# Optimization experiments

Hardware: AMD Instinct MI355X
Metric: run time of the kernel (lower is better)

Reference implementation:

```python
import jax, jax.numpy as jnp
import numpy as np

B = 2          # batch
S = 4096       # byte-level sequence length
D = 512        # d_hidden_bytelevel
BPL = 4        # bytes_per_latent
H = 16         # n_attention_heads
DQK = 64       # d_qkv_bytelevel (== rope d_hidden)
DLAT = 1024    # d_hidden_latent
LQ = S // BPL  # latent sequence length
EPS = 1.1920929e-07  # torch RMSNorm default eps = float32 finfo eps
ROPE_BASE = 10000.0


def _rope(x, pos):
    # x: [B, H, L, DQK], pos: [L] float positions. Half-split rotation.
    half = DQK // 2
    inv_freq = ROPE_BASE ** (-jnp.arange(half, dtype=jnp.float32) / half)  # [half]
    ang = pos[:, None] * inv_freq[None, :]                                 # [L, half]
    cos, sin = jnp.cos(ang), jnp.sin(ang)
    x1, x2 = x[..., :half], x[..., half:]
    return jnp.concatenate([x1 * cos - x2 * sin, x1 * sin + x2 * cos], axis=-1)


def setup_inputs() -> dict:
    key = jax.random.key(0)
    ks = jax.random.split(key, 9)
    s = 0.02
    return {
        "x": jax.random.normal(ks[0], (B, S, D), dtype=jnp.float32),
        "norm_w": jnp.ones((D,), dtype=jnp.float32),
        "wq_w": jax.random.normal(ks[1], (BPL * D, H * DQK), dtype=jnp.float32) * s,
        "wq_b": jax.random.normal(ks[2], (H * DQK,), dtype=jnp.float32) * s,
        "wkv_w": jax.random.normal(ks[3], (D, 2 * H * DQK), dtype=jnp.float32) * s,
        "wkv_b": jax.random.normal(ks[4], (2 * H * DQK,), dtype=jnp.float32) * s,
        "wout_w": jax.random.normal(ks[5], (H * DQK, DLAT), dtype=jnp.float32) * s,
        "wout_b": jax.random.normal(ks[6], (DLAT,), dtype=jnp.float32) * s,
        "wbyp_w": jax.random.normal(ks[7], (BPL * D, DLAT), dtype=jnp.float32) * s,
    }


def reference(x, norm_w, wq_w, wq_b, wkv_w, wkv_b, wout_w, wout_b, wbyp_w):
    # RMSNorm (elementwise affine)
    normalized = x * jax.lax.rsqrt(jnp.mean(x * x, axis=-1, keepdims=True) + EPS) * norm_w
    # merge groups of BPL bytes -> latent query tokens: [B, LQ, BPL*D]
    merged = normalized.reshape(B, LQ, BPL * D)
    # fused Q projection: [B, H, LQ, DQK]
    q = (merged @ wq_w + wq_b).reshape(B, LQ, H, DQK).transpose(0, 2, 1, 3)
    # merged KV projection: split dim first, then heads -> [B, S, 2, H, DQK]
    kv = (normalized @ wkv_w + wkv_b).reshape(B, S, 2, H, DQK)
    k = kv[:, :, 0].transpose(0, 2, 1, 3)  # [B, H, S, DQK]
    v = kv[:, :, 1].transpose(0, 2, 1, 3)
    # strided RoPE for Q (positions i*BPL), unit-stride for K
    q = _rope(q, jnp.arange(LQ, dtype=jnp.float32) * BPL)
    k = _rope(k, jnp.arange(S, dtype=jnp.float32))
    # SDPA (non-causal)
    scores = jnp.einsum('bhqd,bhkd->bhqk', q, k) * (1.0 / np.sqrt(DQK).astype(np.float32))
    attn = jax.nn.softmax(scores, axis=-1)
    attn_out = jnp.einsum('bhqk,bhkd->bhqd', attn, v)
    attn_concat = attn_out.transpose(0, 2, 1, 3).reshape(B, LQ, H * DQK)
    out = attn_concat @ wout_w + wout_b
    # bypass: raw x grouped by BPL, bias-free projection
    bypass = x.reshape(B, LQ, BPL * D) @ wbyp_w
    return out + bypass
```

## Files before the change

### kernel.cpp

```cpp
#include <hip/hip_runtime.h>

using u16 = unsigned short;
using u32 = unsigned int;

typedef __attribute__((ext_vector_type(8))) short bf16x8;
typedef __attribute__((ext_vector_type(8))) unsigned short u16x8;
typedef __attribute__((ext_vector_type(4))) float f32x4;
typedef __attribute__((ext_vector_type(16))) float f32x16;
typedef __attribute__((ext_vector_type(4))) u32 u32x4;

constexpr int Bb   = 2;
constexpr int Ss   = 4096;
constexpr int Dd   = 512;
constexpr int Hh   = 16;
constexpr int DQK  = 64;
constexpr int LQ   = 1024;
constexpr int DLAT = 1024;

#define QSCL 0.18033688011112042f

__device__ __forceinline__ u16 f2bf(float f){
  u32 u = __float_as_uint(f);
  u += 0x7FFFu + ((u >> 16) & 1u);
  return (u16)(u >> 16);
}
__device__ __forceinline__ u32 permpack(float hi, float lo){
  return __builtin_amdgcn_perm(__float_as_uint(hi), __float_as_uint(lo), 0x07060302u);
}

#define GLDS16(gp, lp) \
  __builtin_amdgcn_global_load_lds((const __attribute__((address_space(1))) u32*)(gp), \
                                   (__attribute__((address_space(3))) u32*)(lp), 16, 0, 0)

__global__ __launch_bounds__(256) void rmsnorm_kernel(
    const float* __restrict__ x, const float* __restrict__ w,
    u16* __restrict__ normb, u16* __restrict__ xb)
{
  const int lane = threadIdx.x & 63;
  const int row  = blockIdx.x * 4 + (threadIdx.x >> 6);
  const float4* xr = (const float4*)(x + (size_t)row * Dd);
  float4 a = xr[lane*2], b2 = xr[lane*2 + 1];
  float ss = a.x*a.x + a.y*a.y + a.z*a.z + a.w*a.w
           + b2.x*b2.x + b2.y*b2.y + b2.z*b2.z + b2.w*b2.w;
  #pragma unroll
  for (int off = 1; off < 64; off <<= 1) ss += __shfl_xor(ss, off);
  const float sc = rsqrtf(ss * (1.0f / Dd) + 1.1920929e-07f);
  const int c0 = lane * 8;
  const float4* wr4 = (const float4*)(w + c0);
  float4 w0 = wr4[0], w1 = wr4[1];
  u16x8 nv, xv;
  nv[0]=f2bf(a.x *sc*w0.x); nv[1]=f2bf(a.y *sc*w0.y); nv[2]=f2bf(a.z *sc*w0.z); nv[3]=f2bf(a.w *sc*w0.w);
  nv[4]=f2bf(b2.x*sc*w1.x); nv[5]=f2bf(b2.y*sc*w1.y); nv[6]=f2bf(b2.z*sc*w1.z); nv[7]=f2bf(b2.w*sc*w1.w);
  xv[0]=f2bf(a.x);  xv[1]=f2bf(a.y);  xv[2]=f2bf(a.z);  xv[3]=f2bf(a.w);
  xv[4]=f2bf(b2.x); xv[5]=f2bf(b2.y); xv[6]=f2bf(b2.z); xv[7]=f2bf(b2.w);
  *(u16x8*)(normb + (size_t)row * Dd + c0) = nv;
  *(u16x8*)(xb    + (size_t)row * Dd + c0) = xv;
}

__global__ __launch_bounds__(256) void rope_tab_kernel(float2* __restrict__ tab){
  int i = blockIdx.x * 256 + threadIdx.x;
  int pos = i >> 5, d = i & 31;
  float inv = exp2f(-(float)d * 0.41524101186092028f);
  float ang = (float)pos * inv;
  float s, c;
  sincosf(ang, &s, &c);
  tab[i] = make_float2(c, s);
}

__global__ __launch_bounds__(256) void transpose_cast_kernel(
    const float* __restrict__ W, u16* __restrict__ Wt,
    int N, int ldt, int koff)
{
  __shared__ float t[64][65];
  const int k0 = blockIdx.x * 64, n0 = blockIdx.y * 64;
  const int c = threadIdx.x & 63, r0 = threadIdx.x >> 6;
  #pragma unroll
  for (int i = 0; i < 16; ++i){
    int r = i*4 + r0;
    t[r][c] = W[(size_t)(k0 + r) * N + n0 + c];
  }
  __syncthreads();
  #pragma unroll
  for (int i = 0; i < 16; ++i){
    int r = i*4 + r0;
    Wt[(size_t)(n0 + r) * ldt + koff + k0 + c] = f2bf(t[c][r]);
  }
}

__device__ __forceinline__ void gemm_core64(
    const u16* __restrict__ A, int lda,
    const u16* __restrict__ Bt, int ldb, int kofs,
    int K, int bm0, int bn0, char* lds,
    f32x4 (&acc)[4])
{
  const int tid = threadIdx.x, lane = tid & 63, w = tid >> 6;
  const int l15 = lane & 15, l4 = lane >> 4;

  #pragma unroll
  for (int j = 0; j < 4; ++j) acc[j] = (f32x4){0.f, 0.f, 0.f, 0.f};

  auto stage = [&](int t){
    char* dst = lds + (t % 3) * 16384;
    const int k0 = t * 64;
    #pragma unroll
    for (int i = 0; i < 4; ++i){
      int u = i*256 + tid;
      int row = u >> 3;
      int colb = ((u & 7) * 16) ^ ((row & 7) << 4);
      const u16* src = (row < 64)
        ? A  + (size_t)(bm0 + row) * lda + k0 + (colb >> 1)
        : Bt + (size_t)(bn0 + row - 64) * ldb + kofs + k0 + (colb >> 1);
      GLDS16(src, dst + u*16);
    }
  };

  const int nt = K >> 6;
  stage(0);
  if (nt > 1) stage(1);

  #pragma unroll 1
  for (int t = 0; t < nt; ++t){
    if (t + 1 < nt) { asm volatile("s_waitcnt vmcnt(4)" ::: "memory"); }
    else            { asm volatile("s_waitcnt vmcnt(0)" ::: "memory"); }
    __builtin_amdgcn_sched_barrier(0);
    __builtin_amdgcn_s_barrier();

    const char* kb = lds + (t % 3) * 16384;
    bf16x8 af[2], bf[4][2];
    #pragma unroll
    for (int ks = 0; ks < 2; ++ks){
      const int row = w*16 + l15;
      af[ks] = *(const bf16x8*)(kb + row*128 + ((ks*64 + l4*16) ^ ((row & 7) << 4)));
    }
    #pragma unroll
    for (int j = 0; j < 4; ++j)
      #pragma unroll
      for (int ks = 0; ks < 2; ++ks){
        const int row = 64 + j*16 + l15;
        bf[j][ks] = *(const bf16x8*)(kb + row*128 + ((ks*64 + l4*16) ^ ((row & 7) << 4)));
      }
    asm volatile("s_waitcnt lgkmcnt(0)" ::: "memory");
    __builtin_amdgcn_sched_barrier(0);
    if (t + 2 < nt) stage(t + 2);

    __builtin_amdgcn_s_setprio(1);
    #pragma unroll
    for (int ks = 0; ks < 2; ++ks)
      #pragma unroll
      for (int j = 0; j < 4; ++j)
        acc[j] = __builtin_amdgcn_mfma_f32_16x16x32_bf16(af[ks], bf[j][ks], acc[j], 0, 0, 0);
    __builtin_amdgcn_s_setprio(0);
  }
}

__device__ __forceinline__ void gemm_core256(
    const u16* __restrict__ A, int lda, int ksplit,
    const u16* __restrict__ A2, int lda2,
    const u16* __restrict__ Bt, int ldb,
    int K, int bm0, int bn0, char* lds,
    f32x4 (&acc)[4][4])
{
  const int tid = threadIdx.x, lane = tid & 63, w = tid >> 6;
  const int wr = w >> 1, wc = w & 1;
  const int l15 = lane & 15, l4 = lane >> 4;

  #pragma unroll
  for (int i = 0; i < 4; ++i)
    #pragma unroll
    for (int j = 0; j < 4; ++j) acc[i][j] = (f32x4){0.f, 0.f, 0.f, 0.f};

  auto stage = [&](int t){
    char* dst = lds + (t % 3) * 49152;
    const int k0 = t * 64;
    #pragma unroll
    for (int i = 0; i < 6; ++i){
      int u = i*512 + tid;
      int row = u >> 3;
      int colb = ((u & 7) * 16) ^ ((row & 7) << 4);
      const u16* src;
      if (row < 256){
        if (k0 < ksplit) src = A  + (size_t)(bm0 + row) * lda  + k0 + (colb >> 1);
        else             src = A2 + (size_t)(bm0 + row) * lda2 + (k0 - ksplit) + (colb >> 1);
      } else {
        src = Bt + (size_t)(bn0 + row - 256) * ldb + k0 + (colb >> 1);
      }
      GLDS16(src, dst + u*16);
    }
  };

  const int nt = K >> 6;
  stage(0);
  if (nt > 1) stage(1);

  #pragma unroll 1
  for (int t = 0; t < nt; ++t){
    if (t + 1 < nt) { asm volatile("s_waitcnt vmcnt(6)" ::: "memory"); }
    else            { asm volatile("s_waitcnt vmcnt(0)" ::: "memory"); }
    __builtin_amdgcn_sched_barrier(0);
    __builtin_amdgcn_s_barrier();

    const char* kb = lds + (t % 3) * 49152;
    bf16x8 af[4][2], bf[4][2];
    #pragma unroll
    for (int i = 0; i < 4; ++i)
      #pragma unroll
      for (int ks = 0; ks < 2; ++ks){
        const int row = wr*64 + i*16 + l15;
        af[i][ks] = *(const bf16x8*)(kb + row*128 + ((ks*64 + l4*16) ^ ((row & 7) << 4)));
      }
    #pragma unroll
    for (int j = 0; j < 4; ++j)
      #pragma unroll
      for (int ks = 0; ks < 2; ++ks){
        const int row = 256 + wc*64 + j*16 + l15;
        bf[j][ks] = *(const bf16x8*)(kb + row*128 + ((ks*64 + l4*16) ^ ((row & 7) << 4)));
      }
    asm volatile("s_waitcnt lgkmcnt(0)" ::: "memory");
    __builtin_amdgcn_sched_barrier(0);
    if (t + 2 < nt) stage(t + 2);

    __builtin_amdgcn_s_setprio(1);
    #pragma unroll
    for (int ks = 0; ks < 2; ++ks)
      #pragma unroll
      for (int i = 0; i < 4; ++i)
        #pragma unroll
        for (int j = 0; j < 4; ++j)
          acc[i][j] = __builtin_amdgcn_mfma_f32_16x16x32_bf16(af[i][ks], bf[j][ks], acc[i][j], 0, 0, 0);
    __builtin_amdgcn_s_setprio(0);
  }
}

__global__ __launch_bounds__(512, 1) void qkv_kernel(
    const u16* __restrict__ normb,
    const u16* __restrict__ wtq, const u16* __restrict__ wtkv,
    const float* __restrict__ wq_b, const float* __restrict__ wkv_b,
    const float2* __restrict__ rtab,
    u16* __restrict__ Qb, u16* __restrict__ Kb, u16* __restrict__ Vtb)
{
  __shared__ char lds[147456];
  const int bid = blockIdx.x;
  const int lane = threadIdx.x & 63, w = threadIdx.x >> 6;
  const int wr = w >> 1, wc = w & 1;
  const int ml = (lane >> 4) * 4, nl = lane & 15;
  f32x4 acc[4][4];

  if (bid < 64){
    const int bm0 = (bid & 7) * 256, bn0 = (bid >> 3) * 128;
    gemm_core256(normb, 2048, 2048, normb, 2048, wtq, 2048, 2048, bm0, bn0, lds, acc);
    const int nbase = bn0 + wc*64;
    const int h = nbase >> 6;
    #pragma unroll
    for (int i = 0; i < 4; ++i){
      #pragma unroll
      for (int j = 0; j < 2; ++j){
        const int d1 = j*16 + nl;
        const float b1 = wq_b[nbase + j*16 + nl], b2v = wq_b[nbase + (j+2)*16 + nl];
        #pragma unroll
        for (int r = 0; r < 4; ++r){
          int m = bm0 + wr*64 + i*16 + ml + r;
          int b = m >> 10, lq = m & 1023;
          float x1 = acc[i][j][r] + b1;
          float x2 = acc[i][j+2][r] + b2v;
          float2 cs = rtab[(lq*4)*32 + d1];
          size_t ob = ((size_t)(b*Hh + h) * LQ + lq) * DQK;
          Qb[ob + d1]      = f2bf((x1*cs.x - x2*cs.y) * QSCL);
          Qb[ob + d1 + 32] = f2bf((x1*cs.y + x2*cs.x) * QSCL);
        }
      }
    }
  } else {
    const int t = bid - 64;
    const int bm0 = (t & 31) * 256, bn0 = (t >> 5) * 128;
    gemm_core256(normb, 512, 512, normb, 512, wtkv, 512, 512, bm0, bn0, lds, acc);
    const int nbase = bn0 + wc*64;
    const int kv = nbase >> 10;
    const int h = (nbase & 1023) >> 6;
    #pragma unroll
    for (int i = 0; i < 4; ++i){
      const int m0 = bm0 + wr*64 + i*16 + ml;
      const int b = m0 >> 12, s = m0 & 4095;
      if (kv == 0){
        #pragma unroll
        for (int r = 0; r < 4; ++r){
          size_t ob = ((size_t)(b*Hh + h) * Ss + s + r) * DQK;
          #pragma unroll
          for (int j = 0; j < 2; ++j){
            int d1 = j*16 + nl;
            float x1 = acc[i][j][r]   + wkv_b[nbase + j*16 + nl];
            float x2 = acc[i][j+2][r] + wkv_b[nbase + (j+2)*16 + nl];
            float2 cs = rtab[(s+r)*32 + d1];
            Kb[ob + d1]      = f2bf(x1*cs.x - x2*cs.y);
            Kb[ob + d1 + 32] = f2bf(x1*cs.y + x2*cs.x);
          }
        }
      } else {
        #pragma unroll
        for (int j = 0; j < 4; ++j){
          const int d = j*16 + nl;
          const float bb = wkv_b[nbase + d];
          uint2 pv;
          pv.x = permpack(acc[i][j][1] + bb, acc[i][j][0] + bb);
          pv.y = permpack(acc[i][j][3] + bb, acc[i][j][2] + bb);
          *(uint2*)(Vtb + (((size_t)(b*Hh + h)) * DQK + d) * Ss + s) = pv;
        }
      }
    }
  }
}

__global__ __launch_bounds__(256, 3) void out_kernel(
    const u16* __restrict__ ACb, const u16* __restrict__ xb,
    const u16* __restrict__ wto, const float* __restrict__ wout_b,
    float* __restrict__ outp)
{
  __shared__ char lds[49152];
  const int bm0 = blockIdx.x * 64, bn0 = blockIdx.y * 64;
  const int lane = threadIdx.x & 63, w = threadIdx.x >> 6;
  const int ml = (lane >> 4) * 4, nl = lane & 15;
  f32x4 acc[4], acc2[4];
  gemm_core64(ACb, 1024, wto, 3072, 0,    1024, bm0, bn0, lds, acc);
  __syncthreads();
  gemm_core64(xb,  2048, wto, 3072, 1024, 2048, bm0, bn0, lds, acc2);
  #pragma unroll
  for (int j = 0; j < 4; ++j){
    const int n = bn0 + j*16 + nl;
    const float bb = wout_b[n];
    #pragma unroll
    for (int r = 0; r < 4; ++r){
      int m = bm0 + w*16 + ml + r;
      outp[(size_t)m * DLAT + n] = acc[j][r] + acc2[j][r] + bb;
    }
  }
}

__global__ __launch_bounds__(512, 2) void flash_kernel(
    const u16* __restrict__ Qg, const u16* __restrict__ Kg,
    const u16* __restrict__ Vtg, float* __restrict__ Opart,
    float* __restrict__ lpart)
{
  const int tid = threadIdx.x, lane = tid & 63, w = tid >> 6;
  const int bid = blockIdx.x;
  const int swz = (bid & 7) * 32 + (bid >> 3);
  const int sq = swz & 3, qh = (swz >> 2) & 1, bh = swz >> 3;
  const int sbase = sq * 1024;
  const int l31 = lane & 31, hgl = lane >> 5;

  __shared__ char lds[49152];

  bf16x8 qf[2][4];
  #pragma unroll
  for (int qt = 0; qt < 2; ++qt)
    #pragma unroll
    for (int ks = 0; ks < 4; ++ks)
      qf[qt][ks] = *(const bf16x8*)(Qg + ((size_t)bh*LQ + qh*512 + w*64 + qt*32 + l31) * DQK + ks*16 + hgl*8);

  f32x16 o[2][2];
  #pragma unroll
  for (int qt = 0; qt < 2; ++qt)
    #pragma unroll
    for (int nd = 0; nd < 2; ++nd)
      #pragma unroll
      for (int r = 0; r < 16; ++r) o[qt][nd][r] = 0.f;
  float l_run[2] = {0.f, 0.f};

  auto stage = [&](int t){
    char* dst = lds + (t % 3) * 16384;
    const int s0 = sbase + t * 64;
    #pragma unroll
    for (int i = 0; i < 2; ++i){
      int u = (w*2 + i) * 64 + lane;
      int row = (u >> 3) & 63;
      int colb = ((u & 7) * 16) ^ ((row & 7) << 4);
      const u16* src = (u < 512)
          ? Kg  + ((size_t)bh*Ss  + s0 + row) * DQK + (colb >> 1)
          : Vtg + ((size_t)bh*DQK + row) * Ss + s0  + (colb >> 1);
      GLDS16(src, dst + u*16);
    }
  };

  stage(0);
  stage(1);

  #pragma unroll 1
  for (int t = 0; t < 16; ++t){
    if (t < 15) { asm volatile("s_waitcnt vmcnt(2)" ::: "memory"); }
    else        { asm volatile("s_waitcnt vmcnt(0)" ::: "memory"); }
    __builtin_amdgcn_sched_barrier(0);
    __builtin_amdgcn_s_barrier();

    const char* kb = lds + (t % 3) * 16384;
    bf16x8 kf[2][4], vf[2][4];
    #pragma unroll
    for (int kvt = 0; kvt < 2; ++kvt)
      #pragma unroll
      for (int ks = 0; ks < 4; ++ks){
        const int row = kvt*32 + l31;
        kf[kvt][ks] = *(const bf16x8*)(kb + row*128 + ((ks*32 + hgl*16) ^ ((row & 7) << 4)));
      }
    #pragma unroll
    for (int nd = 0; nd < 2; ++nd)
      #pragma unroll
      for (int k2 = 0; k2 < 4; ++k2){
        const int row = nd*32 + l31;
        vf[nd][k2] = *(const bf16x8*)(kb + 8192 + row*128 + ((k2*32 + hgl*16) ^ ((row & 7) << 4)));
      }
    asm volatile("s_waitcnt lgkmcnt(0)" ::: "memory");
    __builtin_amdgcn_sched_barrier(0);
    if (t < 14) stage(t + 2);

    #pragma unroll
    for (int qt = 0; qt < 2; ++qt){
      f32x16 sc[2];
      #pragma unroll
      for (int kvt = 0; kvt < 2; ++kvt)
        #pragma unroll
        for (int r = 0; r < 16; ++r) sc[kvt][r] = 0.f;
      __builtin_amdgcn_s_setprio(1);
      #pragma unroll
      for (int kvt = 0; kvt < 2; ++kvt)
        #pragma unroll
        for (int ks = 0; ks < 4; ++ks)
          sc[kvt] = __builtin_amdgcn_mfma_f32_32x32x16_bf16(kf[kvt][ks], qf[qt][ks], sc[kvt], 0, 0, 0);
      __builtin_amdgcn_s_setprio(0);

      float s_loc = 0.f;
      u32x4 paw[4];
      #pragma unroll
      for (int kvt = 0; kvt < 2; ++kvt){
        #pragma unroll
        for (int r = 0; r < 16; ++r){
          float p = __builtin_amdgcn_exp2f(sc[kvt][r]);
          sc[kvt][r] = p;
          s_loc += p;
        }
        #pragma unroll
        for (int k2r = 0; k2r < 2; ++k2r){
          u32 a0 = permpack(sc[kvt][k2r*8+1], sc[kvt][k2r*8+0]);
          u32 a1 = permpack(sc[kvt][k2r*8+3], sc[kvt][k2r*8+2]);
          u32 a2 = permpack(sc[kvt][k2r*8+5], sc[kvt][k2r*8+4]);
          u32 a3 = permpack(sc[kvt][k2r*8+7], sc[kvt][k2r*8+6]);
          asm("v_permlane32_swap_b32 %0, %1" : "+v"(a0), "+v"(a2));
          asm("v_permlane32_swap_b32 %0, %1" : "+v"(a1), "+v"(a3));
          const int k2 = kvt*2 + k2r;
          paw[k2][0] = a0; paw[k2][1] = a1;
          paw[k2][2] = a2; paw[k2][3] = a3;
        }
      }
      l_run[qt] += s_loc;

      __builtin_amdgcn_s_setprio(1);
      #pragma unroll
      for (int nd = 0; nd < 2; ++nd)
        #pragma unroll
        for (int k2 = 0; k2 < 4; ++k2)
          o[qt][nd] = __builtin_amdgcn_mfma_f32_32x32x16_bf16(
              __builtin_bit_cast(bf16x8, paw[k2]), vf[nd][k2], o[qt][nd], 0, 0, 0);
      __builtin_amdgcn_s_setprio(0);
    }
  }

  #pragma unroll
  for (int qt = 0; qt < 2; ++qt){
    float lf = l_run[qt] + __shfl_xor(l_run[qt], 32);
    float* Ob = Opart + ((size_t)sq * 32768 + (size_t)bh * 1024) * 64;
    #pragma unroll
    for (int nd = 0; nd < 2; ++nd)
      #pragma unroll
      for (int r = 0; r < 16; ++r){
        int q = qh*512 + w*64 + qt*32 + (r & 3) + 8*(r >> 2) + 4*hgl;
        Ob[(size_t)q * 64 + nd*32 + l31] = o[qt][nd][r];
      }
    if (hgl == 0)
      lpart[(size_t)sq * 32768 + (size_t)bh * 1024 + qh*512 + w*64 + qt*32 + l31] = lf;
  }
}

__global__ __launch_bounds__(256) void merge_kernel(
    const float* __restrict__ Opart, const float* __restrict__ lpart,
    u16* __restrict__ AC)
{
  int idx = blockIdx.x * 256 + threadIdx.x;
  int row = idx >> 3, dg = idx & 7;
  int bh = row >> 10, lq = row & 1023;
  int b = bh >> 4, h = bh & 15;
  float a[8];
  #pragma unroll
  for (int e = 0; e < 8; ++e) a[e] = 0.f;
  float lt = 0.f;
  #pragma unroll
  for (int p = 0; p < 4; ++p){
    const float4* pp = (const float4*)(Opart + ((size_t)p * 32768 + row) * 64 + dg * 8);
    float4 v0 = pp[0], v1 = pp[1];
    a[0]+=v0.x; a[1]+=v0.y; a[2]+=v0.z; a[3]+=v0.w;
    a[4]+=v1.x; a[5]+=v1.y; a[6]+=v1.z; a[7]+=v1.w;
    lt += lpart[(size_t)p * 32768 + row];
  }
  float rl = 1.0f / lt;
  u16x8 r;
  #pragma unroll
  for (int e = 0; e < 8; ++e) r[e] = f2bf(a[e] * rl);
  *(u16x8*)(AC + ((size_t)(b*LQ + lq)) * (Hh*DQK) + h*DQK + dg*8) = r;
}

extern "C" void kernel_launch(void* const* d_in, const int* in_sizes, int n_in,
                              void* d_out, int out_size, void* d_ws, size_t ws_size,
                              hipStream_t stream)
{
  (void)in_sizes; (void)n_in; (void)out_size; (void)ws_size;
  const float* x      = (const float*)d_in[0];
  const float* norm_w = (const float*)d_in[1];
  const float* wq_w   = (const float*)d_in[2];
  const float* wq_b   = (const float*)d_in[3];
  const float* wkv_w  = (const float*)d_in[4];
  const float* wkv_b  = (const float*)d_in[5];
  const float* wout_w = (const float*)d_in[6];
  const float* wout_b = (const float*)d_in[7];
  const float* wbyp_w = (const float*)d_in[8];
  float* outp = (float*)d_out;

  char* p = (char*)d_ws;
  u16* normb = (u16*)p; p += (size_t)8192*512*2;
  u16* xb    = (u16*)p; p += (size_t)8192*512*2;
  u16* wtq   = (u16*)p; p += (size_t)1024*2048*2;
  u16* wtkv  = (u16*)p; p += (size_t)2048*512*2;
  u16* wto   = (u16*)p; p += (size_t)1024*3072*2;
  u16* Qb    = (u16*)p; p += (size_t)32*1024*64*2;
  u16* Kb    = (u16*)p; p += (size_t)32*4096*64*2;
  u16* Vtb   = (u16*)p; p += (size_t)32*64*4096*2;
  u16* ACb   = (u16*)p; p += (size_t)2048*1024*2;
  float2* rtab = (float2*)p; p += (size_t)4096*32*sizeof(float2);
  float* Opart = (float*)p; p += (size_t)4*32768*64*4;
  float* lpart = (float*)p; p += (size_t)4*32768*4;

  rmsnorm_kernel<<<2048, 256, 0, stream>>>(x, norm_w, normb, xb);
  rope_tab_kernel<<<512, 256, 0, stream>>>(rtab);
  transpose_cast_kernel<<<dim3(32,16), 256, 0, stream>>>(wq_w,   wtq,  1024, 2048, 0);
  transpose_cast_kernel<<<dim3(8,32),  256, 0, stream>>>(wkv_w,  wtkv, 2048, 512,  0);
  transpose_cast_kernel<<<dim3(16,16), 256, 0, stream>>>(wout_w, wto,  1024, 3072, 0);
  transpose_cast_kernel<<<dim3(32,16), 256, 0, stream>>>(wbyp_w, wto,  1024, 3072, 1024);

  qkv_kernel<<<576, 512, 0, stream>>>(normb, wtq, wtkv, wq_b, wkv_b, rtab, Qb, Kb, Vtb);
  flash_kernel<<<256, 512, 0, stream>>>(Qb, Kb, Vtb, Opart, lpart);
  merge_kernel<<<1024, 256, 0, stream>>>(Opart, lpart, ACb);
  out_kernel<<<dim3(32,16), 256, 0, stream>>>(ACb, xb, wto, wout_b, outp);
}
```

Baseline: 131.1 us.

## Fuse prep kernels, merge out GEMMs, bf16 partials, reorder flash score MFMAs

Six preprocessing launches (RMSNorm, RoPE table, four weight transpose-casts) become one kernel that branches on block index, which removes launch gaps. The output projection and bypass GEMMs now run as a single K-concatenated GEMM loop, so the accumulator and pipeline are shared. Flash partial outputs are stored in bf16, halving merge traffic at some precision cost. The flash loop computes score MFMAs for both query tiles before loading V fragments, and issues the next K/V prefetch earlier.

```diff
diff --git a/kernel.cpp b/kernel.cpp
--- a/kernel.cpp
+++ b/kernel.cpp
@@ -32,47 +32,11 @@
   __builtin_amdgcn_global_load_lds((const __attribute__((address_space(1))) u32*)(gp), \
                                    (__attribute__((address_space(3))) u32*)(lp), 16, 0, 0)
 
-__global__ __launch_bounds__(256) void rmsnorm_kernel(
-    const float* __restrict__ x, const float* __restrict__ w,
-    u16* __restrict__ normb, u16* __restrict__ xb)
-{
-  const int lane = threadIdx.x & 63;
-  const int row  = blockIdx.x * 4 + (threadIdx.x >> 6);
-  const float4* xr = (const float4*)(x + (size_t)row * Dd);
-  float4 a = xr[lane*2], b2 = xr[lane*2 + 1];
-  float ss = a.x*a.x + a.y*a.y + a.z*a.z + a.w*a.w
-           + b2.x*b2.x + b2.y*b2.y + b2.z*b2.z + b2.w*b2.w;
-  #pragma unroll
-  for (int off = 1; off < 64; off <<= 1) ss += __shfl_xor(ss, off);
-  const float sc = rsqrtf(ss * (1.0f / Dd) + 1.1920929e-07f);
-  const int c0 = lane * 8;
-  const float4* wr4 = (const float4*)(w + c0);
-  float4 w0 = wr4[0], w1 = wr4[1];
-  u16x8 nv, xv;
-  nv[0]=f2bf(a.x *sc*w0.x); nv[1]=f2bf(a.y *sc*w0.y); nv[2]=f2bf(a.z *sc*w0.z); nv[3]=f2bf(a.w *sc*w0.w);
-  nv[4]=f2bf(b2.x*sc*w1.x); nv[5]=f2bf(b2.y*sc*w1.y); nv[6]=f2bf(b2.z*sc*w1.z); nv[7]=f2bf(b2.w*sc*w1.w);
-  xv[0]=f2bf(a.x);  xv[1]=f2bf(a.y);  xv[2]=f2bf(a.z);  xv[3]=f2bf(a.w);
-  xv[4]=f2bf(b2.x); xv[5]=f2bf(b2.y); xv[6]=f2bf(b2.z); xv[7]=f2bf(b2.w);
-  *(u16x8*)(normb + (size_t)row * Dd + c0) = nv;
-  *(u16x8*)(xb    + (size_t)row * Dd + c0) = xv;
-}
-
-__global__ __launch_bounds__(256) void rope_tab_kernel(float2* __restrict__ tab){
-  int i = blockIdx.x * 256 + threadIdx.x;
-  int pos = i >> 5, d = i & 31;
-  float inv = exp2f(-(float)d * 0.41524101186092028f);
-  float ang = (float)pos * inv;
-  float s, c;
-  sincosf(ang, &s, &c);
-  tab[i] = make_float2(c, s);
-}
-
-__global__ __launch_bounds__(256) void transpose_cast_kernel(
+__device__ __forceinline__ void tc_body(
     const float* __restrict__ W, u16* __restrict__ Wt,
-    int N, int ldt, int koff)
-{
-  __shared__ float t[64][65];
-  const int k0 = blockIdx.x * 64, n0 = blockIdx.y * 64;
+    int N, int ldt, int koff, int k0, int n0, float* tbuf)
+{
+  float (*t)[65] = (float(*)[65])tbuf;
   const int c = threadIdx.x & 63, r0 = threadIdx.x >> 6;
   #pragma unroll
   for (int i = 0; i < 16; ++i){
@@ -87,9 +51,65 @@
   }
 }
 
+__global__ __launch_bounds__(256) void prep_kernel(
+    const float* __restrict__ x, const float* __restrict__ norm_w,
+    const float* __restrict__ wq_w, const float* __restrict__ wkv_w,
+    const float* __restrict__ wout_w, const float* __restrict__ wbyp_w,
+    u16* __restrict__ normb, u16* __restrict__ xb,
+    float2* __restrict__ rtab,
+    u16* __restrict__ wtq, u16* __restrict__ wtkv, u16* __restrict__ wto)
+{
+  __shared__ float tbuf[64*65];
+  const int bid = blockIdx.x;
+  if (bid < 2048){
+    const int lane = threadIdx.x & 63;
+    const int row  = bid * 4 + (threadIdx.x >> 6);
+    const float4* xr = (const float4*)(x + (size_t)row * Dd);
+    float4 a = xr[lane*2], b2 = xr[lane*2 + 1];
+    float ss = a.x*a.x + a.y*a.y + a.z*a.z + a.w*a.w
+             + b2.x*b2.x + b2.y*b2.y + b2.z*b2.z + b2.w*b2.w;
+    #pragma unroll
+    for (int off = 1; off < 64; off <<= 1) ss += __shfl_xor(ss, off);
+    const float sc = rsqrtf(ss * (1.0f / Dd) + 1.1920929e-07f);
+    const int c0 = lane * 8;
+    const float4* wr4 = (const float4*)(norm_w + c0);
+    float4 w0 = wr4[0], w1 = wr4[1];
+    u16x8 nv, xv;
+    nv[0]=f2bf(a.x *sc*w0.x); nv[1]=f2bf(a.y *sc*w0.y); nv[2]=f2bf(a.z *sc*w0.z); nv[3]=f2bf(a.w *sc*w0.w);
+    nv[4]=f2bf(b2.x*sc*w1.x); nv[5]=f2bf(b2.y*sc*w1.y); nv[6]=f2bf(b2.z*sc*w1.z); nv[7]=f2bf(b2.w*sc*w1.w);
+    xv[0]=f2bf(a.x);  xv[1]=f2bf(a.y);  xv[2]=f2bf(a.z);  xv[3]=f2bf(a.w);
+    xv[4]=f2bf(b2.x); xv[5]=f2bf(b2.y); xv[6]=f2bf(b2.z); xv[7]=f2bf(b2.w);
+    *(u16x8*)(normb + (size_t)row * Dd + c0) = nv;
+    *(u16x8*)(xb    + (size_t)row * Dd + c0) = xv;
+  } else if (bid < 2560){
+    int i = (bid - 2048) * 256 + threadIdx.x;
+    int pos = i >> 5, d = i & 31;
+    float inv = exp2f(-(float)d * 0.41524101186092028f);
+    float ang = (float)pos * inv;
+    float s, c;
+    sincosf(ang, &s, &c);
+    rtab[i] = make_float2(c, s);
+  } else {
+    int t = bid - 2560;
+    if (t < 512){
+      tc_body(wq_w, wtq, 1024, 2048, 0, (t & 31) * 64, (t >> 5) * 64, tbuf);
+    } else if (t < 768){
+      int u = t - 512;
+      tc_body(wkv_w, wtkv, 2048, 512, 0, (u & 7) * 64, (u >> 3) * 64, tbuf);
+    } else if (t < 1024){
+      int u = t - 768;
+      tc_body(wout_w, wto, 1024, 3072, 0, (u & 15) * 64, (u >> 4) * 64, tbuf);
+    } else {
+      int u = t - 1024;
+      tc_body(wbyp_w, wto, 1024, 3072, 1024, (u & 31) * 64, (u >> 5) * 64, tbuf);
+    }
+  }
+}
+
 __device__ __forceinline__ void gemm_core64(
-    const u16* __restrict__ A, int lda,
-    const u16* __restrict__ Bt, int ldb, int kofs,
+    const u16* __restrict__ A, int lda, int ksplit,
+    const u16* __restrict__ A2, int lda2,
+    const u16* __restrict__ Bt, int ldb,
     int K, int bm0, int bn0, char* lds,
     f32x4 (&acc)[4])
 {
@@ -107,9 +127,13 @@
       int u = i*256 + tid;
       int row = u >> 3;
       int colb = ((u & 7) * 16) ^ ((row & 7) << 4);
-      const u16* src = (row < 64)
-        ? A  + (size_t)(bm0 + row) * lda + k0 + (colb >> 1)
-        : Bt + (size_t)(bn0 + row - 64) * ldb + kofs + k0 + (colb >> 1);
+      const u16* src;
+      if (row < 64){
+        if (k0 < ksplit) src = A  + (size_t)(bm0 + row) * lda  + k0 + (colb >> 1);
+        else             src = A2 + (size_t)(bm0 + row) * lda2 + (k0 - ksplit) + (colb >> 1);
+      } else {
+        src = Bt + (size_t)(bn0 + row - 64) * ldb + k0 + (colb >> 1);
+      }
       GLDS16(src, dst + u*16);
     }
   };
@@ -318,10 +342,8 @@
   const int bm0 = blockIdx.x * 64, bn0 = blockIdx.y * 64;
   const int lane = threadIdx.x & 63, w = threadIdx.x >> 6;
   const int ml = (lane >> 4) * 4, nl = lane & 15;
-  f32x4 acc[4], acc2[4];
-  gemm_core64(ACb, 1024, wto, 3072, 0,    1024, bm0, bn0, lds, acc);
-  __syncthreads();
-  gemm_core64(xb,  2048, wto, 3072, 1024, 2048, bm0, bn0, lds, acc2);
+  f32x4 acc[4];
+  gemm_core64(ACb, 1024, 1024, xb, 2048, wto, 3072, 3072, bm0, bn0, lds, acc);
   #pragma unroll
   for (int j = 0; j < 4; ++j){
     const int n = bn0 + j*16 + nl;
@@ -329,14 +351,14 @@
     #pragma unroll
     for (int r = 0; r < 4; ++r){
       int m = bm0 + w*16 + ml + r;
-      outp[(size_t)m * DLAT + n] = acc[j][r] + acc2[j][r] + bb;
+      outp[(size_t)m * DLAT + n] = acc[j][r] + bb;
     }
   }
 }
 
 __global__ __launch_bounds__(512, 2) void flash_kernel(
     const u16* __restrict__ Qg, const u16* __restrict__ Kg,
-    const u16* __restrict__ Vtg, float* __restrict__ Opart,
+    const u16* __restrict__ Vtg, u16* __restrict__ Opart,
     float* __restrict__ lpart)
 {
   const int tid = threadIdx.x, lane = tid & 63, w = tid >> 6;
@@ -390,7 +412,7 @@
     __builtin_amdgcn_s_barrier();
 
     const char* kb = lds + (t % 3) * 16384;
-    bf16x8 kf[2][4], vf[2][4];
+    bf16x8 kf[2][4];
     #pragma unroll
     for (int kvt = 0; kvt < 2; ++kvt)
       #pragma unroll
@@ -398,6 +420,28 @@
         const int row = kvt*32 + l31;
         kf[kvt][ks] = *(const bf16x8*)(kb + row*128 + ((ks*32 + hgl*16) ^ ((row & 7) << 4)));
       }
+    asm volatile("s_waitcnt lgkmcnt(0)" ::: "memory");
+    __builtin_amdgcn_sched_barrier(0);
+    if (t < 14) stage(t + 2);
+
+    f32x16 sc[2][2];
+    #pragma unroll
+    for (int qt = 0; qt < 2; ++qt)
+      #pragma unroll
+      for (int kvt = 0; kvt < 2; ++kvt)
+        #pragma unroll
+        for (int r = 0; r < 16; ++r) sc[qt][kvt][r] = 0.f;
+    __builtin_amdgcn_s_setprio(1);
+    #pragma unroll
+    for (int qt = 0; qt < 2; ++qt)
+      #pragma unroll
+      for (int kvt = 0; kvt < 2; ++kvt)
+        #pragma unroll
+        for (int ks = 0; ks < 4; ++ks)
+          sc[qt][kvt] = __builtin_amdgcn_mfma_f32_32x32x16_bf16(kf[kvt][ks], qf[qt][ks], sc[qt][kvt], 0, 0, 0);
+    __builtin_amdgcn_s_setprio(0);
+
+    bf16x8 vf[2][4];
     #pragma unroll
     for (int nd = 0; nd < 2; ++nd)
       #pragma unroll
@@ -407,47 +451,35 @@
       }
     asm volatile("s_waitcnt lgkmcnt(0)" ::: "memory");
     __builtin_amdgcn_sched_barrier(0);
-    if (t < 14) stage(t + 2);
 
     #pragma unroll
     for (int qt = 0; qt < 2; ++qt){
-      f32x16 sc[2];
       #pragma unroll
       for (int kvt = 0; kvt < 2; ++kvt)
         #pragma unroll
-        for (int r = 0; r < 16; ++r) sc[kvt][r] = 0.f;
-      __builtin_amdgcn_s_setprio(1);
+        for (int r = 0; r < 16; ++r)
+          sc[qt][kvt][r] = __builtin_amdgcn_exp2f(sc[qt][kvt][r]);
+      f32x16 es = sc[qt][0] + sc[qt][1];
+      float a0 = es[0]+es[8],  a1 = es[1]+es[9],  a2 = es[2]+es[10], a3 = es[3]+es[11];
+      float a4 = es[4]+es[12], a5 = es[5]+es[13], a6 = es[6]+es[14], a7 = es[7]+es[15];
+      float b0 = a0+a4, b1 = a1+a5, b2 = a2+a6, b3 = a3+a7;
+      l_run[qt] += (b0+b1) + (b2+b3);
+
+      u32x4 paw[4];
       #pragma unroll
       for (int kvt = 0; kvt < 2; ++kvt)
         #pragma unroll
-        for (int ks = 0; ks < 4; ++ks)
-          sc[kvt] = __builtin_amdgcn_mfma_f32_32x32x16_bf16(kf[kvt][ks], qf[qt][ks], sc[kvt], 0, 0, 0);
-      __builtin_amdgcn_s_setprio(0);
-
-      float s_loc = 0.f;
-      u32x4 paw[4];
-      #pragma unroll
-      for (int kvt = 0; kvt < 2; ++kvt){
-        #pragma unroll
-        for (int r = 0; r < 16; ++r){
-          float p = __builtin_amdgcn_exp2f(sc[kvt][r]);
-          sc[kvt][r] = p;
-          s_loc += p;
+        for (int k2r = 0; k2r < 2; ++k2r){
+          u32 w0 = permpack(sc[qt][kvt][k2r*8+1], sc[qt][kvt][k2r*8+0]);
+          u32 w1 = permpack(sc[qt][kvt][k2r*8+3], sc[qt][kvt][k2r*8+2]);
+          u32 w2 = permpack(sc[qt][kvt][k2r*8+5], sc[qt][kvt][k2r*8+4]);
+          u32 w3 = permpack(sc[qt][kvt][k2r*8+7], sc[qt][kvt][k2r*8+6]);
+          asm("v_permlane32_swap_b32 %0, %1" : "+v"(w0), "+v"(w2));
+          asm("v_permlane32_swap_b32 %0, %1" : "+v"(w1), "+v"(w3));
+          const int k2 = kvt*2 + k2r;
+          paw[k2][0] = w0; paw[k2][1] = w1;
+          paw[k2][2] = w2; paw[k2][3] = w3;
         }
-        #pragma unroll
-        for (int k2r = 0; k2r < 2; ++k2r){
-          u32 a0 = permpack(sc[kvt][k2r*8+1], sc[kvt][k2r*8+0]);
-          u32 a1 = permpack(sc[kvt][k2r*8+3], sc[kvt][k2r*8+2]);
-          u32 a2 = permpack(sc[kvt][k2r*8+5], sc[kvt][k2r*8+4]);
-          u32 a3 = permpack(sc[kvt][k2r*8+7], sc[kvt][k2r*8+6]);
-          asm("v_permlane32_swap_b32 %0, %1" : "+v"(a0), "+v"(a2));
-          asm("v_permlane32_swap_b32 %0, %1" : "+v"(a1), "+v"(a3));
-          const int k2 = kvt*2 + k2r;
-          paw[k2][0] = a0; paw[k2][1] = a1;
-          paw[k2][2] = a2; paw[k2][3] = a3;
-        }
-      }
-      l_run[qt] += s_loc;
 
       __builtin_amdgcn_s_setprio(1);
       #pragma unroll
@@ -463,13 +495,13 @@
   #pragma unroll
   for (int qt = 0; qt < 2; ++qt){
     float lf = l_run[qt] + __shfl_xor(l_run[qt], 32);
-    float* Ob = Opart + ((size_t)sq * 32768 + (size_t)bh * 1024) * 64;
+    u16* Ob = Opart + ((size_t)sq * 32768 + (size_t)bh * 1024) * 64;
     #pragma unroll
     for (int nd = 0; nd < 2; ++nd)
       #pragma unroll
       for (int r = 0; r < 16; ++r){
         int q = qh*512 + w*64 + qt*32 + (r & 3) + 8*(r >> 2) + 4*hgl;
-        Ob[(size_t)q * 64 + nd*32 + l31] = o[qt][nd][r];
+        Ob[(size_t)q * 64 + nd*32 + l31] = f2bf(o[qt][nd][r]);
       }
     if (hgl == 0)
       lpart[(size_t)sq * 32768 + (size_t)bh * 1024 + qh*512 + w*64 + qt*32 + l31] = lf;
@@ -477,7 +509,7 @@
 }
 
 __global__ __launch_bounds__(256) void merge_kernel(
-    const float* __restrict__ Opart, const float* __restrict__ lpart,
+    const u16* __restrict__ Opart, const float* __restrict__ lpart,
     u16* __restrict__ AC)
 {
   int idx = blockIdx.x * 256 + threadIdx.x;
@@ -490,10 +522,10 @@
   float lt = 0.f;
   #pragma unroll
   for (int p = 0; p < 4; ++p){
-    const float4* pp = (const float4*)(Opart + ((size_t)p * 32768 + row) * 64 + dg * 8);
-    float4 v0 = pp[0], v1 = pp[1];
-    a[0]+=v0.x; a[1]+=v0.y; a[2]+=v0.z; a[3]+=v0.w;
-    a[4]+=v1.x; a[5]+=v1.y; a[6]+=v1.z; a[7]+=v1.w;
+    u16x8 v = *(const u16x8*)(Opart + ((size_t)p * 32768 + row) * 64 + dg * 8);
+    #pragma unroll
+    for (int e = 0; e < 8; ++e)
+      a[e] += __uint_as_float((u32)v[e] << 16);
     lt += lpart[(size_t)p * 32768 + row];
   }
   float rl = 1.0f / lt;
@@ -530,16 +562,11 @@
   u16* Vtb   = (u16*)p; p += (size_t)32*64*4096*2;
   u16* ACb   = (u16*)p; p += (size_t)2048*1024*2;
   float2* rtab = (float2*)p; p += (size_t)4096*32*sizeof(float2);
-  float* Opart = (float*)p; p += (size_t)4*32768*64*4;
+  u16* Opart = (u16*)p; p += (size_t)4*32768*64*2;
   float* lpart = (float*)p; p += (size_t)4*32768*4;
 
-  rmsnorm_kernel<<<2048, 256, 0, stream>>>(x, norm_w, normb, xb);
-  rope_tab_kernel<<<512, 256, 0, stream>>>(rtab);
-  transpose_cast_kernel<<<dim3(32,16), 256, 0, stream>>>(wq_w,   wtq,  1024, 2048, 0);
-  transpose_cast_kernel<<<dim3(8,32),  256, 0, stream>>>(wkv_w,  wtkv, 2048, 512,  0);
-  transpose_cast_kernel<<<dim3(16,16), 256, 0, stream>>>(wout_w, wto,  1024, 3072, 0);
-  transpose_cast_kernel<<<dim3(32,16), 256, 0, stream>>>(wbyp_w, wto,  1024, 3072, 1024);
-
+  prep_kernel<<<4096, 256, 0, stream>>>(x, norm_w, wq_w, wkv_w, wout_w, wbyp_w,
+                                        normb, xb, rtab, wtq, wtkv, wto);
   qkv_kernel<<<576, 512, 0, stream>>>(normb, wtq, wtkv, wq_b, wkv_b, rtab, Qb, Kb, Vtb);
   flash_kernel<<<256, 512, 0, stream>>>(Qb, Kb, Vtb, Opart, lpart);
   merge_kernel<<<1024, 256, 0, stream>>>(Opart, lpart, ACb);
```

Result: faster. 120.9 us (-7.8%).
